# Kernel tuning notes

Measured on AMD Instinct MI355X. Metric: run time of the kernel, lower is better.

The kernel has to match this reference:

```python
import jax, jax.numpy as jnp
import numpy as np

BS, NUM_RELS, NUM_NODES, EMB = 8, 16, 512, 256


def setup_inputs() -> dict:
    key = jax.random.key(0)
    k1, k2, k3, k4 = jax.random.split(key, 4)
    features = jax.random.normal(k1, (BS, NUM_NODES, EMB), dtype=jnp.float32)
    adjacency = jax.random.uniform(k2, (BS, NUM_RELS, NUM_NODES, NUM_NODES), dtype=jnp.float32)
    # xavier_uniform bounds
    bound = float(np.sqrt(6.0 / (EMB + EMB)))
    W_r = jax.random.uniform(k3, (NUM_RELS, EMB, EMB), minval=-bound, maxval=bound, dtype=jnp.float32)
    W_0 = jax.random.uniform(k4, (EMB, EMB), minval=-bound, maxval=bound, dtype=jnp.float32)
    return {"features": features, "adjacency": adjacency, "W_r": W_r, "W_0": W_0}


def reference(features, adjacency, W_r, W_0):
    # msg[b,r,n,d] = sum_m adjacency[b,r,n,m] * features[b,m,d]
    msg = jnp.einsum('brnm,bmd->brnd', adjacency, features)
    # per-relation projection then sum over relations: [b,n,h]
    features_1 = jnp.einsum('brnd,rdh->bnh', msg, W_r)
    features_2 = jnp.einsum('bnd,dh->bnh', features, W_0)
    return jax.nn.relu(features_1 + features_2)
```

## Files before the change

### kernel.cpp

```cpp
#include <hip/hip_runtime.h>
#include <hip/hip_bf16.h>

#define BS   8
#define NREL 16
#define NN   512
#define EMB  256

typedef float f32x4 __attribute__((ext_vector_type(4)));
typedef short s16x8 __attribute__((ext_vector_type(8)));

__device__ __forceinline__ unsigned short f2bf_bits(float f) {
    union { float f; unsigned u; } v; v.f = f;
    unsigned r = (v.u + 0x7FFFu + ((v.u >> 16) & 1u)) >> 16;
    return (unsigned short)r;
}

__device__ __forceinline__ unsigned short f2bf_hw(float f) {
    union { __hip_bfloat16 h; unsigned short u; } v;
    v.h = __float2bfloat16(f);
    return v.u;
}

__global__ __launch_bounds__(256) void k0_prep(
        const float* __restrict__ Wr, const float* __restrict__ W0,
        const float* __restrict__ F,
        unsigned short* __restrict__ wT, unsigned short* __restrict__ Fbf) {
    int bid = blockIdx.x;
    if (bid < 1088) {
        __shared__ float tile[32][33];
        int rel = bid / 64;
        int t   = bid % 64;
        int d0  = (t & 7) * 32;
        int h0  = (t >> 3) * 32;
        int tx  = threadIdx.x & 31;
        int ty  = threadIdx.x >> 5;
        const float* src = (rel < NREL) ? (Wr + rel * (EMB * EMB)) : W0;
#pragma unroll
        for (int k = 0; k < 4; ++k) {
            int d = d0 + ty + k * 8;
            tile[ty + k * 8][tx] = src[d * EMB + h0 + tx];
        }
        __syncthreads();
#pragma unroll
        for (int k = 0; k < 4; ++k) {
            int h = h0 + ty + k * 8;
            wT[(rel * EMB + h) * EMB + d0 + tx] = f2bf_bits(tile[tx][ty + k * 8]);
        }
    } else {
        long i = ((long)(bid - 1088) * 256 + threadIdx.x) * 8;
        f32x4 x0 = *(const f32x4*)(F + i);
        f32x4 x1 = *(const f32x4*)(F + i + 4);
        s16x8 v;
        v[0] = (short)f2bf_bits(x0[0]); v[1] = (short)f2bf_bits(x0[1]);
        v[2] = (short)f2bf_bits(x0[2]); v[3] = (short)f2bf_bits(x0[3]);
        v[4] = (short)f2bf_bits(x1[0]); v[5] = (short)f2bf_bits(x1[1]);
        v[6] = (short)f2bf_bits(x1[2]); v[7] = (short)f2bf_bits(x1[3]);
        *(s16x8*)(Fbf + i) = v;
    }
}

__global__ __launch_bounds__(256) void k1_fw(
        const unsigned short* __restrict__ Fbf, const unsigned short* __restrict__ wT,
        unsigned short* __restrict__ FW, float* __restrict__ F2f) {
    int bid = blockIdx.x;
    int b   = bid & 7;
    int q   = bid >> 3;
    int rel = q % 17;
    int mt  = q / 17;
    int tid = threadIdx.x;
    int w   = tid >> 6;
    int l   = tid & 63;
    int lg  = l >> 4;
    int lr  = l & 15;

    int h0 = w * 64;
    int m0 = mt * 64;

    const unsigned short* wt = wT + rel * (EMB * EMB) + lg * 8;
    const unsigned short* Fb = Fbf + (long)b * (NN * EMB) + lg * 8;

    f32x4 acc[4][4];
#pragma unroll
    for (int i = 0; i < 4; ++i)
#pragma unroll
        for (int j = 0; j < 4; ++j) acc[i][j] = (f32x4){0.f, 0.f, 0.f, 0.f};

    s16x8 afr[2][4], bfr[2][4];
#pragma unroll
    for (int hi = 0; hi < 4; ++hi)
        afr[0][hi] = *(const s16x8*)(wt + (h0 + hi * 16 + lr) * EMB);
#pragma unroll
    for (int bi = 0; bi < 4; ++bi)
        bfr[0][bi] = *(const s16x8*)(Fb + (m0 + bi * 16 + lr) * EMB);

#pragma unroll
    for (int kk = 0; kk < 8; ++kk) {
        int cur = kk & 1, nxt = cur ^ 1;
        if (kk < 7) {
            int ko = (kk + 1) * 32;
#pragma unroll
            for (int hi = 0; hi < 4; ++hi)
                afr[nxt][hi] = *(const s16x8*)(wt + (h0 + hi * 16 + lr) * EMB + ko);
#pragma unroll
            for (int bi = 0; bi < 4; ++bi)
                bfr[nxt][bi] = *(const s16x8*)(Fb + (m0 + bi * 16 + lr) * EMB + ko);
        }
#pragma unroll
        for (int hi = 0; hi < 4; ++hi)
#pragma unroll
            for (int bi = 0; bi < 4; ++bi)
                acc[hi][bi] = __builtin_amdgcn_mfma_f32_16x16x32_bf16(
                    afr[cur][hi], bfr[cur][bi], acc[hi][bi], 0, 0, 0);
    }

#pragma unroll
    for (int hi = 0; hi < 4; ++hi) {
#pragma unroll
        for (int bi = 0; bi < 4; ++bi) {
            int m  = m0 + bi * 16 + lr;
            int kg = m >> 3, ko = m & 7;
#pragma unroll
            for (int j = 0; j < 4; ++j) {
                int h = h0 + hi * 16 + lg * 4 + j;
                if (rel < NREL)
                    FW[(long)((b * 16 + rel) * 64 + kg) * 2048 + h * 8 + ko] =
                        f2bf_bits(acc[hi][bi][j]);
                else
                    F2f[((long)b * NN + m) * EMB + h] = acc[hi][bi][j];
            }
        }
    }
}

__global__ __launch_bounds__(512, 2) void k2_main(
        const float* __restrict__ adj, const unsigned short* __restrict__ FW,
        float* __restrict__ part) {
    __shared__ unsigned short Blds[2][16384];
    int bid = blockIdx.x;
    int b   = bid & 7;
    int t   = bid >> 3;
    int nt  = t & 3;
    int rg  = t >> 2;
    int tid = threadIdx.x;
    int w   = tid >> 6;
    int l   = tid & 63;
    int lg  = l >> 4, lr = l & 15;
    int wc  = w & 1;
    int hh  = (w >> 1) & 1;
    int rh  = w >> 2;

    int nrow0 = nt * 128 + rh * 64;
    int h0    = hh * 128;

    f32x4 acc[4][8];
#pragma unroll
    for (int ar = 0; ar < 4; ++ar)
#pragma unroll
        for (int f = 0; f < 8; ++f) acc[ar][f] = (f32x4){0.f, 0.f, 0.f, 0.f};

    const float* adjb =
        adj + (((long)(b * 16 + rg * 2)) * NN + nrow0 + lr) * NN + lg * 8;
    const unsigned short* fwb = FW + (long)(b * 16 + rg * 2) * 131072;

    s16x8 fwr[4];
    f32x4 ax[2][4], ay[2][4];

#define POFF(p) ((long)((p) >> 3) * 131072 + ((p) & 7) * 16384)

    {
        const unsigned short* s = fwb + POFF(0) + tid * 8;
#pragma unroll
        for (int c = 0; c < 4; ++c) fwr[c] = *(const s16x8*)(s + c * 4096);
#pragma unroll
        for (int c = 0; c < 4; ++c)
            *(s16x8*)(&Blds[0][c * 4096 + tid * 8]) = fwr[c];
    }
    {
#pragma unroll
        for (int ar = 0; ar < 4; ++ar) {
            const float* p = adjb + ar * (16 * NN) + wc * 32;
            ax[0][ar] = *(const f32x4*)p;
            ay[0][ar] = *(const f32x4*)(p + 4);
        }
    }
    {
        const unsigned short* s = fwb + POFF(1) + tid * 8;
#pragma unroll
        for (int c = 0; c < 4; ++c) fwr[c] = *(const s16x8*)(s + c * 4096);
    }
    asm volatile("s_waitcnt lgkmcnt(0)" ::: "memory");
    __builtin_amdgcn_sched_barrier(0);
    __builtin_amdgcn_s_barrier();
    asm volatile("" ::: "memory");

#pragma unroll
    for (int i = 0; i < 16; ++i) {
        if (i + 1 < 16) {
            int sl = 2 * (i + 1) + wc;
            long ao = (long)(sl >> 4) * (NN * NN) + (sl & 15) * 32;
#pragma unroll
            for (int ar = 0; ar < 4; ++ar) {
                const float* p = adjb + ar * (16 * NN) + ao;
                if (((i + 1) & 1) == 0) {
                    ax[0][ar] = *(const f32x4*)p; ay[0][ar] = *(const f32x4*)(p + 4);
                } else {
                    ax[1][ar] = *(const f32x4*)p; ay[1][ar] = *(const f32x4*)(p + 4);
                }
            }
        }

        s16x8 afr[4];
#pragma unroll
        for (int ar = 0; ar < 4; ++ar) {
            f32x4 x0 = ax[i & 1][ar], x1 = ay[i & 1][ar];
            s16x8 a;
            a[0] = (short)f2bf_hw(x0[0]); a[1] = (short)f2bf_hw(x0[1]);
            a[2] = (short)f2bf_hw(x0[2]); a[3] = (short)f2bf_hw(x0[3]);
            a[4] = (short)f2bf_hw(x1[0]); a[5] = (short)f2bf_hw(x1[1]);
            a[6] = (short)f2bf_hw(x1[2]); a[7] = (short)f2bf_hw(x1[3]);
            afr[ar] = a;
        }

        const unsigned short* bl = &Blds[i & 1][wc * 8192 + lg * 2048];
#pragma unroll
        for (int f = 0; f < 8; ++f) {
            s16x8 bf = *(const s16x8*)(bl + (h0 + f * 16 + lr) * 8);
            acc[0][f] = __builtin_amdgcn_mfma_f32_16x16x32_bf16(afr[0], bf, acc[0][f], 0, 0, 0);
            acc[1][f] = __builtin_amdgcn_mfma_f32_16x16x32_bf16(afr[1], bf, acc[1][f], 0, 0, 0);
            acc[2][f] = __builtin_amdgcn_mfma_f32_16x16x32_bf16(afr[2], bf, acc[2][f], 0, 0, 0);
            acc[3][f] = __builtin_amdgcn_mfma_f32_16x16x32_bf16(afr[3], bf, acc[3][f], 0, 0, 0);
        }
        asm volatile("" ::: "memory");

        if (i + 1 < 16) {
            unsigned short* dst = &Blds[(i + 1) & 1][tid * 8];
#pragma unroll
            for (int c = 0; c < 4; ++c) *(s16x8*)(dst + c * 4096) = fwr[c];
            if (i + 2 < 16) {
                const unsigned short* s = fwb + POFF(i + 2) + tid * 8;
#pragma unroll
                for (int c = 0; c < 4; ++c) fwr[c] = *(const s16x8*)(s + c * 4096);
            }
            asm volatile("s_waitcnt lgkmcnt(0)" ::: "memory");
            __builtin_amdgcn_sched_barrier(0);
            __builtin_amdgcn_s_barrier();
            asm volatile("" ::: "memory");
        }
    }
#undef POFF

    float* lf = (float*)Blds;
    float* pp = part + ((long)rg * BS + b) * (NN * EMB);
    int wid2 = w >> 1;
#pragma unroll
    for (int g = 0; g < 2; ++g) {
        __syncthreads();
        if (wc == 1) {
#pragma unroll
            for (int aq = 0; aq < 2; ++aq)
#pragma unroll
                for (int f = 0; f < 8; ++f)
#pragma unroll
                    for (int j = 0; j < 4; ++j)
                        lf[wid2 * 4096 + ((aq * 8 + f) * 4 + j) * 64 + l] =
                            acc[g * 2 + aq][f][j];
        }
        __syncthreads();
        if (wc == 0) {
#pragma unroll
            for (int aq = 0; aq < 2; ++aq) {
                int ar = g * 2 + aq;
#pragma unroll
                for (int f = 0; f < 8; ++f) {
                    int h = h0 + f * 16 + lr;
#pragma unroll
                    for (int j = 0; j < 4; ++j) {
                        int n = nrow0 + ar * 16 + lg * 4 + j;
                        float v = acc[ar][f][j] +
                                  lf[wid2 * 4096 + ((aq * 8 + f) * 4 + j) * 64 + l];
                        pp[(long)n * EMB + h] = v;
                    }
                }
            }
        }
    }
}

__global__ __launch_bounds__(256) void k3_reduce(
        const float* __restrict__ part, const float* __restrict__ F2f,
        float* __restrict__ out) {
    const long PS = (long)BS * NN * EMB;
    long i = ((long)blockIdx.x * 256 + threadIdx.x) * 4;
    f32x4 s = *(const f32x4*)(part + i);
#pragma unroll
    for (int rg = 1; rg < 8; ++rg)
        s += *(const f32x4*)(part + i + (long)rg * PS);
    s += *(const f32x4*)(F2f + i);
    f32x4 r;
#pragma unroll
    for (int j = 0; j < 4; ++j) r[j] = s[j] > 0.f ? s[j] : 0.f;
    *(f32x4*)(out + i) = r;
}

extern "C" void kernel_launch(void* const* d_in, const int* in_sizes, int n_in,
                              void* d_out, int out_size, void* d_ws, size_t ws_size,
                              hipStream_t stream) {
    const float* F   = (const float*)d_in[0];
    const float* adj = (const float*)d_in[1];
    const float* Wr  = (const float*)d_in[2];
    const float* W0  = (const float*)d_in[3];
    float* out = (float*)d_out;

    unsigned short* wT  = (unsigned short*)d_ws;
    unsigned short* Fbf = wT + 17 * 256 * 256;
    unsigned short* FW  = Fbf + (long)8 * 512 * 256;
    float* F2f  = (float*)(FW + (long)8 * 16 * 64 * 2048);
    float* part = F2f + (long)8 * 512 * 256;

    k0_prep<<<1600, 256, 0, stream>>>(Wr, W0, F, wT, Fbf);
    k1_fw<<<1088, 256, 0, stream>>>(Fbf, wT, FW, F2f);
    k2_main<<<256, 512, 0, stream>>>(adj, FW, part);
    k3_reduce<<<1024, 256, 0, stream>>>(part, F2f, out);
}
```

Measured before the change: 110.2 us.

## Restructure k2_main to smaller blocks with direct global-to-LDS staging

The main GEMM kernel now runs 512 blocks of 256 threads, each covering 64 rows instead of 128. The K split across wave pairs is removed, and with it the LDS cross-wave reduction in the epilogue. FW tiles are staged into LDS with global_load_lds, which skips the register round-trip, and each loop step now handles one 32-wide K slice. The aim is better occupancy and a lighter epilogue. In exchange there are twice as many barriers per block, and each B tile loaded into LDS is reused by fewer rows.

```diff
diff --git a/kernel.cpp b/kernel.cpp
--- a/kernel.cpp
+++ b/kernel.cpp
@@ -9,6 +9,9 @@
 typedef float f32x4 __attribute__((ext_vector_type(4)));
 typedef short s16x8 __attribute__((ext_vector_type(8)));
 
+#define GLOBAL_AS __attribute__((address_space(1)))
+#define LDS_AS    __attribute__((address_space(3)))
+
 __device__ __forceinline__ unsigned short f2bf_bits(float f) {
     union { float f; unsigned u; } v; v.f = f;
     unsigned r = (v.u + 0x7FFFu + ((v.u >> 16) & 1u)) >> 16;
@@ -19,6 +22,11 @@
     union { __hip_bfloat16 h; unsigned short u; } v;
     v.h = __float2bfloat16(f);
     return v.u;
+}
+
+__device__ __forceinline__ void stage16(const void* g, void* l) {
+    __builtin_amdgcn_global_load_lds((const GLOBAL_AS unsigned int*)g,
+                                     (LDS_AS unsigned int*)l, 16, 0, 0);
 }
 
 __global__ __launch_bounds__(256) void k0_prep(
@@ -132,29 +140,28 @@
     }
 }
 
-__global__ __launch_bounds__(512, 2) void k2_main(
+__global__ __launch_bounds__(256, 2) void k2_main(
         const float* __restrict__ adj, const unsigned short* __restrict__ FW,
         float* __restrict__ part) {
-    __shared__ unsigned short Blds[2][16384];
+    __shared__ unsigned short Blds[2][8192];
     int bid = blockIdx.x;
     int b   = bid & 7;
     int t   = bid >> 3;
-    int nt  = t & 3;
-    int rg  = t >> 2;
+    int nt  = t & 7;
+    int rg  = t >> 3;
     int tid = threadIdx.x;
     int w   = tid >> 6;
     int l   = tid & 63;
     int lg  = l >> 4, lr = l & 15;
-    int wc  = w & 1;
-    int hh  = (w >> 1) & 1;
-    int rh  = w >> 2;
-
-    int nrow0 = nt * 128 + rh * 64;
+    int rh  = w >> 1;
+    int hh  = w & 1;
+
+    int nrow0 = nt * 64 + rh * 32;
     int h0    = hh * 128;
 
-    f32x4 acc[4][8];
-#pragma unroll
-    for (int ar = 0; ar < 4; ++ar)
+    f32x4 acc[2][8];
+#pragma unroll
+    for (int ar = 0; ar < 2; ++ar)
 #pragma unroll
         for (int f = 0; f < 8; ++f) acc[ar][f] = (f32x4){0.f, 0.f, 0.f, 0.f};
 
@@ -162,57 +169,44 @@
         adj + (((long)(b * 16 + rg * 2)) * NN + nrow0 + lr) * NN + lg * 8;
     const unsigned short* fwb = FW + (long)(b * 16 + rg * 2) * 131072;
 
-    s16x8 fwr[4];
-    f32x4 ax[2][4], ay[2][4];
-
-#define POFF(p) ((long)((p) >> 3) * 131072 + ((p) & 7) * 16384)
+    f32x4 ax[2][2], ay[2][2];
+
+#define SOFF(sl) ((long)((sl) >> 4) * 131072 + ((sl) & 15) * 8192)
 
     {
-        const unsigned short* s = fwb + POFF(0) + tid * 8;
-#pragma unroll
-        for (int c = 0; c < 4; ++c) fwr[c] = *(const s16x8*)(s + c * 4096);
-#pragma unroll
-        for (int c = 0; c < 4; ++c)
-            *(s16x8*)(&Blds[0][c * 4096 + tid * 8]) = fwr[c];
-    }
-    {
-#pragma unroll
-        for (int ar = 0; ar < 4; ++ar) {
-            const float* p = adjb + ar * (16 * NN) + wc * 32;
-            ax[0][ar] = *(const f32x4*)p;
-            ay[0][ar] = *(const f32x4*)(p + 4);
-        }
-    }
-    {
-        const unsigned short* s = fwb + POFF(1) + tid * 8;
-#pragma unroll
-        for (int c = 0; c < 4; ++c) fwr[c] = *(const s16x8*)(s + c * 4096);
-    }
-    asm volatile("s_waitcnt lgkmcnt(0)" ::: "memory");
-    __builtin_amdgcn_sched_barrier(0);
-    __builtin_amdgcn_s_barrier();
-    asm volatile("" ::: "memory");
-
-#pragma unroll
-    for (int i = 0; i < 16; ++i) {
-        if (i + 1 < 16) {
-            int sl = 2 * (i + 1) + wc;
-            long ao = (long)(sl >> 4) * (NN * NN) + (sl & 15) * 32;
-#pragma unroll
-            for (int ar = 0; ar < 4; ++ar) {
+        const unsigned short* src = fwb + SOFF(0) + tid * 8;
+        unsigned short* dst = &Blds[0][tid * 8];
+#pragma unroll
+        for (int c = 0; c < 4; ++c) stage16(src + c * 2048, dst + c * 2048);
+    }
+#pragma unroll
+    for (int ar = 0; ar < 2; ++ar) {
+        const float* p = adjb + ar * (16 * NN);
+        ax[0][ar] = *(const f32x4*)p;
+        ay[0][ar] = *(const f32x4*)(p + 4);
+    }
+    __syncthreads();
+
+#pragma unroll
+    for (int s = 0; s < 32; ++s) {
+        if (s + 1 < 32) {
+            const unsigned short* src = fwb + SOFF(s + 1) + tid * 8;
+            unsigned short* dst = &Blds[(s + 1) & 1][tid * 8];
+#pragma unroll
+            for (int c = 0; c < 4; ++c) stage16(src + c * 2048, dst + c * 2048);
+            long ao = (long)((s + 1) >> 4) * (NN * NN) + ((s + 1) & 15) * 32;
+#pragma unroll
+            for (int ar = 0; ar < 2; ++ar) {
                 const float* p = adjb + ar * (16 * NN) + ao;
-                if (((i + 1) & 1) == 0) {
-                    ax[0][ar] = *(const f32x4*)p; ay[0][ar] = *(const f32x4*)(p + 4);
-                } else {
-                    ax[1][ar] = *(const f32x4*)p; ay[1][ar] = *(const f32x4*)(p + 4);
-                }
+                ax[(s + 1) & 1][ar] = *(const f32x4*)p;
+                ay[(s + 1) & 1][ar] = *(const f32x4*)(p + 4);
             }
         }
 
-        s16x8 afr[4];
-#pragma unroll
-        for (int ar = 0; ar < 4; ++ar) {
-            f32x4 x0 = ax[i & 1][ar], x1 = ay[i & 1][ar];
+        s16x8 afr[2];
+#pragma unroll
+        for (int ar = 0; ar < 2; ++ar) {
+            f32x4 x0 = ax[s & 1][ar], x1 = ay[s & 1][ar];
             s16x8 a;
             a[0] = (short)f2bf_hw(x0[0]); a[1] = (short)f2bf_hw(x0[1]);
             a[2] = (short)f2bf_hw(x0[2]); a[3] = (short)f2bf_hw(x0[3]);
@@ -221,66 +215,28 @@
             afr[ar] = a;
         }
 
-        const unsigned short* bl = &Blds[i & 1][wc * 8192 + lg * 2048];
+        const unsigned short* bl = &Blds[s & 1][lg * 2048];
 #pragma unroll
         for (int f = 0; f < 8; ++f) {
             s16x8 bf = *(const s16x8*)(bl + (h0 + f * 16 + lr) * 8);
             acc[0][f] = __builtin_amdgcn_mfma_f32_16x16x32_bf16(afr[0], bf, acc[0][f], 0, 0, 0);
             acc[1][f] = __builtin_amdgcn_mfma_f32_16x16x32_bf16(afr[1], bf, acc[1][f], 0, 0, 0);
-            acc[2][f] = __builtin_amdgcn_mfma_f32_16x16x32_bf16(afr[2], bf, acc[2][f], 0, 0, 0);
-            acc[3][f] = __builtin_amdgcn_mfma_f32_16x16x32_bf16(afr[3], bf, acc[3][f], 0, 0, 0);
-        }
-        asm volatile("" ::: "memory");
-
-        if (i + 1 < 16) {
-            unsigned short* dst = &Blds[(i + 1) & 1][tid * 8];
-#pragma unroll
-            for (int c = 0; c < 4; ++c) *(s16x8*)(dst + c * 4096) = fwr[c];
-            if (i + 2 < 16) {
-                const unsigned short* s = fwb + POFF(i + 2) + tid * 8;
-#pragma unroll
-                for (int c = 0; c < 4; ++c) fwr[c] = *(const s16x8*)(s + c * 4096);
-            }
-            asm volatile("s_waitcnt lgkmcnt(0)" ::: "memory");
-            __builtin_amdgcn_sched_barrier(0);
-            __builtin_amdgcn_s_barrier();
-            asm volatile("" ::: "memory");
-        }
-    }
-#undef POFF
-
-    float* lf = (float*)Blds;
+        }
+
+        __syncthreads();
+    }
+#undef SOFF
+
     float* pp = part + ((long)rg * BS + b) * (NN * EMB);
-    int wid2 = w >> 1;
-#pragma unroll
-    for (int g = 0; g < 2; ++g) {
-        __syncthreads();
-        if (wc == 1) {
-#pragma unroll
-            for (int aq = 0; aq < 2; ++aq)
-#pragma unroll
-                for (int f = 0; f < 8; ++f)
-#pragma unroll
-                    for (int j = 0; j < 4; ++j)
-                        lf[wid2 * 4096 + ((aq * 8 + f) * 4 + j) * 64 + l] =
-                            acc[g * 2 + aq][f][j];
-        }
-        __syncthreads();
-        if (wc == 0) {
-#pragma unroll
-            for (int aq = 0; aq < 2; ++aq) {
-                int ar = g * 2 + aq;
-#pragma unroll
-                for (int f = 0; f < 8; ++f) {
-                    int h = h0 + f * 16 + lr;
-#pragma unroll
-                    for (int j = 0; j < 4; ++j) {
-                        int n = nrow0 + ar * 16 + lg * 4 + j;
-                        float v = acc[ar][f][j] +
-                                  lf[wid2 * 4096 + ((aq * 8 + f) * 4 + j) * 64 + l];
-                        pp[(long)n * EMB + h] = v;
-                    }
-                }
+#pragma unroll
+    for (int ar = 0; ar < 2; ++ar) {
+#pragma unroll
+        for (int f = 0; f < 8; ++f) {
+            int h = h0 + f * 16 + lr;
+#pragma unroll
+            for (int j = 0; j < 4; ++j) {
+                int n = nrow0 + ar * 16 + lg * 4 + j;
+                pp[(long)n * EMB + h] = acc[ar][f][j];
             }
         }
     }
@@ -319,6 +275,6 @@
 
     k0_prep<<<1600, 256, 0, stream>>>(Wr, W0, F, wT, Fbf);
     k1_fw<<<1088, 256, 0, stream>>>(Fbf, wT, FW, F2f);
-    k2_main<<<256, 512, 0, stream>>>(adj, FW, part);
+    k2_main<<<512, 256, 0, stream>>>(adj, FW, part);
     k3_reduce<<<1024, 256, 0, stream>>>(part, F2f, out);
 }
```

Result: slower. 121.8 us (+10.5%).
